# Optimization experiments

Measured on AMD Instinct MI355X. Metric: run time of the kernel, lower is better.

Reference implementation:

```python
import jax, jax.numpy as jnp
import numpy as np

DIM_INPUT = 100000
DIM_LATENT = 128
NNZ = 819200
BATCH = 16384


def setup_inputs() -> dict:
    key = jax.random.key(0)
    k1, k2, k3, k4, k5 = jax.random.split(key, 5)
    vals = jax.random.uniform(k1, (NNZ,), dtype=jnp.float32)
    row_idx = jnp.sort(jax.random.randint(k2, (NNZ,), 0, BATCH, dtype=jnp.int32))
    col_idx = jax.random.randint(k3, (NNZ,), 0, DIM_INPUT, dtype=jnp.int32)
    # learned parameters (match torch init: w0 zeros, w/v randn)
    w0 = jnp.zeros((1,), dtype=jnp.float32)
    w = jax.random.normal(k4, (DIM_INPUT,), dtype=jnp.float32)
    v = jax.random.normal(k5, (DIM_INPUT, DIM_LATENT), dtype=jnp.float32)
    return {"vals": vals, "row_idx": row_idx, "col_idx": col_idx,
            "batch": BATCH, "w0": w0, "w": w, "v": v}


def reference(vals, row_idx, col_idx, batch, w0, w, v):
    # x is a sparse [batch, dim_input] matrix in COO form (row_idx, col_idx, vals).
    # linear term: w0 + x @ w
    linear = w0[0] + jax.ops.segment_sum(vals * w[col_idx], row_idx,
                                         num_segments=batch)
    # gather latent rows once: [nnz, K]
    v_rows = v[col_idx]
    weighted = vals[:, None] * v_rows                      # [nnz, K]
    xv = jax.ops.segment_sum(weighted, row_idx, num_segments=batch)       # [B, K]
    x_v_sq = jax.ops.segment_sum(weighted * v_rows, row_idx,
                                 num_segments=batch)       # x @ (v**2): [B, K]
    interaction = 0.5 * (jnp.sum(xv * xv, axis=1) - jnp.sum(x_v_sq, axis=1))
    return linear + interaction
```

## Files before the change

kernel.cpp:

```cpp
#include <hip/hip_runtime.h>

#define FM_NNZ   819200
#define FM_BATCH 16384
#define FM_DIM   100000
#define FM_K     128
#define NB_SHIFT 12
#define NBUCK    25
#define UNR      4


static __device__ __forceinline__ uint32_t f2bf(float f) {
    uint32_t u = __float_as_uint(f);
    return (u + 0x7fffu + ((u >> 16) & 1u)) >> 16;
}

__global__ __launch_bounds__(256) void cvt_kernel(const float* __restrict__ v,
                                                  uint32_t* __restrict__ vb) {
    const float4* __restrict__ v4 = (const float4*)v;
    uint2* __restrict__ o = (uint2*)vb;
    const int n = (FM_DIM * FM_K) / 4;
    for (int i = blockIdx.x * blockDim.x + threadIdx.x; i < n;
         i += gridDim.x * blockDim.x) {
        const float4 x = v4[i];
        uint2 r;
        r.x = f2bf(x.x) | (f2bf(x.y) << 16);
        r.y = f2bf(x.z) | (f2bf(x.w) << 16);
        o[i] = r;
    }
}


__global__ __launch_bounds__(256, 4) void fm_fwd_kernel(
    const float* __restrict__ vals,
    const int*   __restrict__ row_idx,
    const int*   __restrict__ col_idx,
    const float* __restrict__ w0,
    const float* __restrict__ w_,
    const uint32_t* __restrict__ vb,
    float*       __restrict__ out)
{
    __shared__ uint2 lists[4][2][128];

    const int wave = threadIdx.x >> 6;
    const int lane = threadIdx.x & 63;
    const int grp  = lane >> 4;
    const int ql   = lane & 15;
    const int wid  = blockIdx.x * 4 + wave;
    const int row0 = 2 * wid;

    int s[3];
    #pragma unroll
    for (int q = 0; q < 3; ++q) {
        const int key = row0 + q;
        int lo = 0, hi = FM_NNZ;
        while (lo < hi) {
            const int mid = (lo + hi) >> 1;
            if (row_idx[mid] < key) lo = mid + 1; else hi = mid;
        }
        s[q] = lo;
    }
    const int s0 = s[0], s1 = s[1], s2 = s[2];

    int cA, cB, cC, cD;  float aA, aB, aC, aD;  int bA, bB, bC, bD;
    {
        int idx, ic; bool ok;
        idx = s0 + lane;      ok = idx < s1; ic = min(idx, FM_NNZ - 1);
        cA = col_idx[ic]; aA = ok ? vals[ic] : 0.f; bA = ok ? (cA >> NB_SHIFT) : 127;
        idx = s0 + 64 + lane; ok = idx < s1; ic = min(idx, FM_NNZ - 1);
        cB = col_idx[ic]; aB = ok ? vals[ic] : 0.f; bB = ok ? (cB >> NB_SHIFT) : 127;
        idx = s1 + lane;      ok = idx < s2; ic = min(idx, FM_NNZ - 1);
        cC = col_idx[ic]; aC = ok ? vals[ic] : 0.f; bC = ok ? (cC >> NB_SHIFT) : 127;
        idx = s1 + 64 + lane; ok = idx < s2; ic = min(idx, FM_NNZ - 1);
        cD = col_idx[ic]; aD = ok ? vals[ic] : 0.f; bD = ok ? (cD >> NB_SHIFT) : 127;
    }

    float lin0 = aA * w_[cA] + aB * w_[cB];
    float lin1 = aC * w_[cC] + aD * w_[cD];

    const unsigned long long lt = (1ull << lane) - 1ull;
    int total0, total1;
    {
        int posA = -1, posB = -1, run = 0;
        for (int p = 0; p < NBUCK; ++p) {
            const unsigned long long mA = __ballot(bA == p);
            const unsigned long long mB = __ballot(bB == p);
            const int nA = __popcll(mA);
            if (bA == p) posA = run + __popcll(mA & lt);
            if (bB == p) posB = run + nA + __popcll(mB & lt);
            run += nA + __popcll(mB);
        }
        total0 = run;
        if (posA >= 0) lists[wave][0][posA] = make_uint2((uint32_t)cA, __float_as_uint(aA));
        if (posB >= 0) lists[wave][0][posB] = make_uint2((uint32_t)cB, __float_as_uint(aB));
    }
    {
        int posC = -1, posD = -1, run = 0;
        for (int p = 0; p < NBUCK; ++p) {
            const unsigned long long mC = __ballot(bC == p);
            const unsigned long long mD = __ballot(bD == p);
            const int nC = __popcll(mC);
            if (bC == p) posC = run + __popcll(mC & lt);
            if (bD == p) posD = run + nC + __popcll(mD & lt);
            run += nC + __popcll(mD);
        }
        total1 = run;
        if (posC >= 0) lists[wave][1][posC] = make_uint2((uint32_t)cC, __float_as_uint(aC));
        if (posD >= 0) lists[wave][1][posD] = make_uint2((uint32_t)cD, __float_as_uint(aD));
    }
    __syncthreads();

    const uint4* __restrict__ vb4 = (const uint4*)vb;

    float xv[8], sq[8];
    float part0, part1;

#define ROWWALK(r, total, partr)                                              \
    {                                                                         \
        _Pragma("unroll")                                                     \
        for (int d = 0; d < 8; ++d) { xv[d] = 0.f; sq[d] = 0.f; }             \
        for (int i = 0; i < (total); i += 4 * UNR) {                          \
            uint2 ca[UNR];                                                    \
            uint4 vv[UNR];                                                    \
            _Pragma("unroll")                                                 \
            for (int u = 0; u < UNR; ++u) {                                   \
                const int e = min(i + 4 * u + grp, (total) - 1);              \
                ca[u] = lists[wave][r][e];       \
            }                                                                 \
            _Pragma("unroll")                                                 \
            for (int u = 0; u < UNR; ++u) {                                   \
                vv[u] = vb4[(size_t)ca[u].x * 16 + ql];        \
            }                                                                 \
            _Pragma("unroll")                                                 \
            for (int u = 0; u < UNR; ++u) {                                   \
                const float aj = (i + 4 * u + grp < (total))                  \
                                     ? __uint_as_float(ca[u].y) : 0.f;        \
                const uint32_t wd[4] = {vv[u].x, vv[u].y, vv[u].z, vv[u].w};  \
                _Pragma("unroll")                                             \
                for (int q2 = 0; q2 < 4; ++q2) {                              \
                    const float vlo = __uint_as_float(wd[q2] << 16);          \
                    const float vhi = __uint_as_float(wd[q2] & 0xffff0000u);  \
                    const float tl = aj * vlo, th = aj * vhi;                 \
                    xv[2*q2]   += tl;                                         \
                    xv[2*q2+1] += th;                                         \
                    sq[2*q2]   = fmaf(tl, vlo, sq[2*q2]);                     \
                    sq[2*q2+1] = fmaf(th, vhi, sq[2*q2+1]);                   \
                }                                                             \
            }                                                                 \
        }                                                                     \
        float px = 0.f, sqs = 0.f;                                            \
        _Pragma("unroll")                                                     \
        for (int d = 0; d < 8; ++d) {                                         \
            float t = xv[d];                                                  \
            t += __shfl_xor(t, 16);                                           \
            t += __shfl_xor(t, 32);                \
            px = fmaf(t, t, px);                                              \
            sqs += sq[d];                                                     \
        }                                                                     \
        partr = ((lane < 16) ? px : 0.f) - sqs;    \
    }

    ROWWALK(0, total0, part0)
    ROWWALK(1, total1, part1)
#undef ROWWALK

    #pragma unroll
    for (int off = 32; off > 0; off >>= 1) {
        part0 += __shfl_down(part0, off);
        part1 += __shfl_down(part1, off);
        lin0  += __shfl_down(lin0,  off);
        lin1  += __shfl_down(lin1,  off);
    }
    if (lane == 0) {
        const float bias = w0[0];
        out[row0]     = bias + lin0 + 0.5f * part0;
        out[row0 + 1] = bias + lin1 + 0.5f * part1;
    }
}

extern "C" void kernel_launch(void* const* d_in, const int* in_sizes, int n_in,
                              void* d_out, int out_size, void* d_ws, size_t ws_size,
                              hipStream_t stream) {
    const float* vals    = (const float*)d_in[0];
    const int*   row_idx = (const int*)  d_in[1];
    const int*   col_idx = (const int*)  d_in[2];
    const float* w0      = (const float*)d_in[4];
    const float* w       = (const float*)d_in[5];
    const float* v       = (const float*)d_in[6];
    float*       out     = (float*)d_out;
    uint32_t*    vb      = (uint32_t*)d_ws;

    cvt_kernel<<<1024, 256, 0, stream>>>(v, vb);
    fm_fwd_kernel<<<FM_BATCH / 8, 256, 0, stream>>>(
        vals, row_idx, col_idx, w0, w, vb, out);
}
```

Before: 167.5 us.

## Precompute per-column squared norms and stage gathered bf16 rows via global_load_lds

The prep kernel now also computes the fp32 squared norm of each latent row and packs it with w into a float2 table. This turns the x@(v^2) term into a per-nonzero scalar lookup, so the inner loop no longer needs the squared accumulations. The row walk now copies the gathered bf16 latent rows straight into LDS with global_load_lds and a full vmcnt wait each batch. Each lane owns two dims, which removes the cross-group shuffle reduction, and the occupancy hint rises to 6 waves. The risks are serialized load/wait stalls with no overlap between batches, and extra LDS reads per nonzero.

```diff
diff --git a/kernel.cpp b/kernel.cpp
--- a/kernel.cpp
+++ b/kernel.cpp
@@ -6,40 +6,46 @@
 #define FM_K     128
 #define NB_SHIFT 12
 #define NBUCK    25
-#define UNR      4
-
+#define SB       16
 
 static __device__ __forceinline__ uint32_t f2bf(float f) {
     uint32_t u = __float_as_uint(f);
     return (u + 0x7fffu + ((u >> 16) & 1u)) >> 16;
 }
 
-__global__ __launch_bounds__(256) void cvt_kernel(const float* __restrict__ v,
-                                                  uint32_t* __restrict__ vb) {
-    const float4* __restrict__ v4 = (const float4*)v;
-    uint2* __restrict__ o = (uint2*)vb;
-    const int n = (FM_DIM * FM_K) / 4;
-    for (int i = blockIdx.x * blockDim.x + threadIdx.x; i < n;
-         i += gridDim.x * blockDim.x) {
-        const float4 x = v4[i];
-        uint2 r;
-        r.x = f2bf(x.x) | (f2bf(x.y) << 16);
-        r.y = f2bf(x.z) | (f2bf(x.w) << 16);
-        o[i] = r;
-    }
+static __device__ __forceinline__ void llds16(const uint32_t* g, uint32_t* l) {
+    __builtin_amdgcn_global_load_lds(
+        (const __attribute__((address_space(1))) uint32_t*)g,
+        (__attribute__((address_space(3))) uint32_t*)l, 16, 0, 0);
+}
+
+__global__ __launch_bounds__(256) void prep_kernel(
+    const float* __restrict__ v, const float* __restrict__ w_,
+    uint32_t* __restrict__ vb, float2* __restrict__ wn)
+{
+    const int wave = threadIdx.x >> 6, lane = threadIdx.x & 63;
+    const int c = blockIdx.x * 4 + wave;
+    if (c >= FM_DIM) return;
+    const float2 x = ((const float2*)v)[(size_t)c * 64 + lane];
+    vb[(size_t)c * 64 + lane] = f2bf(x.x) | (f2bf(x.y) << 16);
+    float s = x.x * x.x + x.y * x.y;
+    #pragma unroll
+    for (int off = 32; off > 0; off >>= 1) s += __shfl_down(s, off);
+    if (lane == 0) wn[c] = make_float2(w_[c], s);
 }
 
 
-__global__ __launch_bounds__(256, 4) void fm_fwd_kernel(
+__global__ __launch_bounds__(256, 6) void fm_fwd_kernel(
     const float* __restrict__ vals,
     const int*   __restrict__ row_idx,
     const int*   __restrict__ col_idx,
     const float* __restrict__ w0,
-    const float* __restrict__ w_,
+    const float2* __restrict__ wn,
     const uint32_t* __restrict__ vb,
     float*       __restrict__ out)
 {
-    __shared__ uint2 lists[4][2][128];
+    __shared__ uint2    lists[4][2][128];
+    __shared__ uint32_t stage[4][SB * 64];
 
     const int wave = threadIdx.x >> 6;
     const int lane = threadIdx.x & 63;
@@ -74,8 +80,11 @@
         cD = col_idx[ic]; aD = ok ? vals[ic] : 0.f; bD = ok ? (cD >> NB_SHIFT) : 127;
     }
 
-    float lin0 = aA * w_[cA] + aB * w_[cB];
-    float lin1 = aC * w_[cC] + aD * w_[cD];
+    const float2 wnA = wn[cA], wnB = wn[cB], wnC = wn[cC], wnD = wn[cD];
+    float lin0 = aA * wnA.x + aB * wnB.x;
+    float lin1 = aC * wnC.x + aD * wnD.x;
+    float sqs0 = aA * wnA.y + aB * wnB.y;
+    float sqs1 = aC * wnC.y + aD * wnD.y;
 
     const unsigned long long lt = (1ull << lane) - 1ull;
     int total0, total1;
@@ -109,58 +118,39 @@
     }
     __syncthreads();
 
-    const uint4* __restrict__ vb4 = (const uint4*)vb;
-
-    float xv[8], sq[8];
     float part0, part1;
 
-#define ROWWALK(r, total, partr)                                              \
+#define ROWWALK(r, total, partr, sqsr)                                        \
     {                                                                         \
-        _Pragma("unroll")                                                     \
-        for (int d = 0; d < 8; ++d) { xv[d] = 0.f; sq[d] = 0.f; }             \
-        for (int i = 0; i < (total); i += 4 * UNR) {                          \
-            uint2 ca[UNR];                                                    \
-            uint4 vv[UNR];                                                    \
+        float xvl = 0.f, xvh = 0.f;                                           \
+        uint32_t* st = &stage[wave][0];                                       \
+        for (int i = 0; i < (total); i += SB) {                               \
             _Pragma("unroll")                                                 \
-            for (int u = 0; u < UNR; ++u) {                                   \
+            for (int u = 0; u < 4; ++u) {                                     \
                 const int e = min(i + 4 * u + grp, (total) - 1);              \
-                ca[u] = lists[wave][r][e];       \
+                const uint2 ca = lists[wave][r][e];   \
+                llds16(vb + (size_t)ca.x * 64 + ql * 4, st + u * 256);        \
             }                                                                 \
+            asm volatile("s_waitcnt vmcnt(0)" ::: "memory");                  \
             _Pragma("unroll")                                                 \
-            for (int u = 0; u < UNR; ++u) {                                   \
-                vv[u] = vb4[(size_t)ca[u].x * 16 + ql];        \
-            }                                                                 \
-            _Pragma("unroll")                                                 \
-            for (int u = 0; u < UNR; ++u) {                                   \
-                const float aj = (i + 4 * u + grp < (total))                  \
-                                     ? __uint_as_float(ca[u].y) : 0.f;        \
-                const uint32_t wd[4] = {vv[u].x, vv[u].y, vv[u].z, vv[u].w};  \
-                _Pragma("unroll")                                             \
-                for (int q2 = 0; q2 < 4; ++q2) {                              \
-                    const float vlo = __uint_as_float(wd[q2] << 16);          \
-                    const float vhi = __uint_as_float(wd[q2] & 0xffff0000u);  \
-                    const float tl = aj * vlo, th = aj * vhi;                 \
-                    xv[2*q2]   += tl;                                         \
-                    xv[2*q2+1] += th;                                         \
-                    sq[2*q2]   = fmaf(tl, vlo, sq[2*q2]);                     \
-                    sq[2*q2+1] = fmaf(th, vhi, sq[2*q2+1]);                   \
-                }                                                             \
+            for (int eb = 0; eb < SB; ++eb) {                                 \
+                const int e = i + eb;                                         \
+                const float av = __uint_as_float(                             \
+                    lists[wave][r][min(e, (total) - 1)].y);                   \
+                const float aj = (e < (total)) ? av : 0.f;                    \
+                const uint32_t u32 =                                          \
+                    st[(eb >> 2) * 256 + (eb & 3) * 64 + lane];               \
+                const float vlo = __uint_as_float(u32 << 16);                 \
+                const float vhi = __uint_as_float(u32 & 0xffff0000u);         \
+                xvl = fmaf(aj, vlo, xvl);                                     \
+                xvh = fmaf(aj, vhi, xvh);                                     \
             }                                                                 \
         }                                                                     \
-        float px = 0.f, sqs = 0.f;                                            \
-        _Pragma("unroll")                                                     \
-        for (int d = 0; d < 8; ++d) {                                         \
-            float t = xv[d];                                                  \
-            t += __shfl_xor(t, 16);                                           \
-            t += __shfl_xor(t, 32);                \
-            px = fmaf(t, t, px);                                              \
-            sqs += sq[d];                                                     \
-        }                                                                     \
-        partr = ((lane < 16) ? px : 0.f) - sqs;    \
+        partr = xvl * xvl + xvh * xvh - sqsr;                                 \
     }
 
-    ROWWALK(0, total0, part0)
-    ROWWALK(1, total1, part1)
+    ROWWALK(0, total0, part0, sqs0)
+    ROWWALK(1, total1, part1, sqs1)
 #undef ROWWALK
 
     #pragma unroll
@@ -187,9 +177,11 @@
     const float* w       = (const float*)d_in[5];
     const float* v       = (const float*)d_in[6];
     float*       out     = (float*)d_out;
-    uint32_t*    vb      = (uint32_t*)d_ws;
 
-    cvt_kernel<<<1024, 256, 0, stream>>>(v, vb);
+    uint32_t* vb = (uint32_t*)d_ws;
+    float2*   wn = (float2*)((char*)d_ws + (size_t)FM_DIM * 64 * 4);
+
+    prep_kernel<<<(FM_DIM + 3) / 4, 256, 0, stream>>>(v, w, vb, wn);
     fm_fwd_kernel<<<FM_BATCH / 8, 256, 0, stream>>>(
-        vals, row_idx, col_idx, w0, w, vb, out);
+        vals, row_idx, col_idx, w0, wn, vb, out);
 }
```

New measurement: 173.0 us. 1.03x slower.
